# Performance work log

Hardware: AMD Instinct MI355X
Metric: run time of the kernel (lower is better)

Reference implementation:

```python
import jax, jax.numpy as jnp
import numpy as np

N_NODES = 50000
N_EDGES = 800000
D_FEAT = 96


def setup_inputs() -> dict:
    key = jax.random.key(0)
    kx, ks, kd = jax.random.split(key, 3)
    x = jax.random.normal(kx, (N_NODES, D_FEAT), dtype=jnp.float32)
    src = jax.random.randint(ks, (N_EDGES,), 0, N_NODES, dtype=jnp.int64)
    dst = jax.random.randint(kd, (N_EDGES,), 0, N_NODES, dtype=jnp.int64)
    return {"x": x, "src": src, "dst": dst}


def reference(x, src, dst):
    n = x.shape[0]
    ones = jnp.ones(src.shape[0], dtype=x.dtype)
    # out-degree: edges leaving each node (src side)
    out_deg = jnp.clip(jax.ops.segment_sum(ones, src, num_segments=n), 1.0, None)
    # in-degree: edges arriving at each node (dst side)
    in_deg = jnp.clip(jax.ops.segment_sum(ones, dst, num_segments=n), 1.0, None)
    # pre-scale by out-degree^{-1/2}
    xs = x * (out_deg ** -0.5)[:, None]
    # copy_u + sum aggregation: sum messages from src into dst
    agg = jax.ops.segment_sum(xs[src], dst, num_segments=n)
    # post-scale by in-degree^{-1/2}
    return agg * (in_deg ** -0.5)[:, None]
```

## Files before the change

kernel.cpp:

```cpp
#include <hip/hip_runtime.h>


#define D_FEAT 96
#define CAP 64
#define PART_SHIFT 8
#define PNODES 256
#define NP_MAX 256
#define EPB 4096
#define EREG 4
#define PTHREADS 1024
#define OVF_CAP 8192

__device__ __forceinline__ unsigned short f2bf_rne(float f) {
    unsigned u = __float_as_uint(f);
    unsigned r = (u >> 16) & 1u;
    u += 0x7fffu + r;
    return (unsigned short)(u >> 16);
}


__global__ __launch_bounds__(PTHREADS) void partition_kernel(
        const int* __restrict__ src, const int* __restrict__ dst,
        int n_edges, int np, int stride,
        int* __restrict__ pcur_d, int* __restrict__ pcur_s,
        unsigned* __restrict__ pbuf_d, unsigned short* __restrict__ pbuf_s,
        int* __restrict__ ctr,
        int* __restrict__ povf_d, int* __restrict__ sovf_d) {
    __shared__ int hcd[NP_MAX], hcs[NP_MAX];
    __shared__ int bd[NP_MAX], bs_[NP_MAX];
    __shared__ int od[NP_MAX], os_[NP_MAX];
    const int base = blockIdx.x * EPB;

    for (int i = threadIdx.x; i < NP_MAX; i += PTHREADS) {
        hcd[i] = 0; hcs[i] = 0; od[i] = 0; os_[i] = 0;
    }
    __syncthreads();

    unsigned v[EREG];
    #pragma unroll
    for (int k = 0; k < EREG; ++k) {
        int i = base + (int)threadIdx.x + (k << 10);
        if (i < n_edges) {
            int s = src[i], d = dst[i];
            unsigned pv = (unsigned)d | ((unsigned)s << 16);
            v[k] = pv;
            atomicAdd(&hcd[d >> PART_SHIFT], 1);
            atomicAdd(&hcs[s >> PART_SHIFT], 1);
        }
    }
    __syncthreads();

    for (int p = threadIdx.x; p < np; p += PTHREADS) {
        int cd = hcd[p];
        bd[p] = cd ? atomicAdd(&pcur_d[p], cd) : 0;
        int cs = hcs[p];
        bs_[p] = cs ? atomicAdd(&pcur_s[p], cs) : 0;
    }
    __syncthreads();

    #pragma unroll
    for (int k = 0; k < EREG; ++k) {
        int i = base + (int)threadIdx.x + (k << 10);
        if (i < n_edges) {
            unsigned pv = v[k];
            int d = (int)(pv & 0xffffu);
            int s = (int)(pv >> 16);
            int pd = d >> PART_SHIFT;
            int j = bd[pd] + atomicAdd(&od[pd], 1);
            if (j < stride) pbuf_d[(size_t)pd * stride + j] = pv;
            else { int k2 = atomicAdd(&ctr[1], 1); if (k2 < OVF_CAP) povf_d[k2] = (int)pv; }
            int ps = s >> PART_SHIFT;
            int j2 = bs_[ps] + atomicAdd(&os_[ps], 1);
            if (j2 < stride) pbuf_s[(size_t)ps * stride + j2] = (unsigned short)s;
            else { int k3 = atomicAdd(&ctr[2], 1); if (k3 < OVF_CAP) sovf_d[k3] = s; }
        }
    }
}


__global__ __launch_bounds__(PTHREADS) void bincnt_kernel(
        const unsigned* __restrict__ pbuf_d, const int* __restrict__ pcur_d,
        const unsigned short* __restrict__ pbuf_s, const int* __restrict__ pcur_s,
        int stride, int n_nodes,
        const float* __restrict__ x, unsigned* __restrict__ xs,
        int* __restrict__ cursor, int* __restrict__ out_cnt,
        unsigned short* __restrict__ slots,
        int* __restrict__ ctr,
        const int* __restrict__ povf_d, const int* __restrict__ sovf_d,
        int* __restrict__ ovf_d) {
    __shared__ unsigned short lslots[PNODES * CAP];
    __shared__ int lcnt[PNODES];
    __shared__ int lout[PNODES];
    const int b = blockIdx.x;
    const int nbase = b << PART_SHIFT;
    const int nloc = min(PNODES, n_nodes - nbase);

    for (int i = threadIdx.x; i < PNODES; i += PTHREADS) { lcnt[i] = 0; lout[i] = 0; }
    __syncthreads();

    int n = pcur_d[b]; if (n > stride) n = stride;
    for (int i = threadIdx.x; i < n; i += PTHREADS) {
        unsigned pv = pbuf_d[(size_t)b * stride + i];
        int dl = (int)(pv & 0xffu);
        int s  = (int)(pv >> 16);
        int pos = atomicAdd(&lcnt[dl], 1);
        if (pos < CAP) lslots[dl * CAP + pos] = (unsigned short)s;
        else { int k = atomicAdd(&ctr[0], 1); if (k < OVF_CAP) ovf_d[k] = (int)pv; }
    }
    int n2 = pcur_s[b]; if (n2 > stride) n2 = stride;
    for (int i = threadIdx.x; i < n2; i += PTHREADS) {
        int s = (int)pbuf_s[(size_t)b * stride + i];
        atomicAdd(&lout[s & (PNODES - 1)], 1);
    }
    int npv = ctr[1];
    if (npv > 0) {
        if (npv > OVF_CAP) npv = OVF_CAP;
        for (int i = threadIdx.x; i < npv; i += PTHREADS) {
            unsigned pv = (unsigned)povf_d[i];
            int d = (int)(pv & 0xffffu);
            if ((d >> PART_SHIFT) == b) {
                int dl = d & (PNODES - 1);
                int pos = atomicAdd(&lcnt[dl], 1);
                if (pos < CAP) lslots[dl * CAP + pos] = (unsigned short)(pv >> 16);
                else { int k = atomicAdd(&ctr[0], 1); if (k < OVF_CAP) ovf_d[k] = (int)pv; }
            }
        }
    }
    int nsv = ctr[2];
    if (nsv > 0) {
        if (nsv > OVF_CAP) nsv = OVF_CAP;
        for (int i = threadIdx.x; i < nsv; i += PTHREADS) {
            int s = sovf_d[i];
            if ((s >> PART_SHIFT) == b) atomicAdd(&lout[s & (PNODES - 1)], 1);
        }
    }
    __syncthreads();

    for (int i = threadIdx.x; i < nloc; i += PTHREADS) {
        cursor[nbase + i]  = lcnt[i];
        out_cnt[nbase + i] = lout[i];
    }
    const unsigned* ls = (const unsigned*)lslots;
    unsigned* gs = (unsigned*)slots + (size_t)nbase * (CAP / 2);
    const int ncopy = nloc * (CAP / 2);
    for (int i = threadIdx.x; i < ncopy; i += PTHREADS) gs[i] = ls[i];

    const int ntot = nloc * 24;
    for (int i = threadIdx.x; i < ntot; i += PTHREADS) {
        int nd = i / 24;
        int j  = i - nd * 24;
        int c  = lout[nd];
        float w = rsqrtf((float)(c < 1 ? 1 : c));
        float4 vv = ((const float4*)(x + (size_t)(nbase + nd) * D_FEAT))[j];
        unsigned lo0 = f2bf_rne(vv.x * w), hi0 = f2bf_rne(vv.y * w);
        unsigned lo1 = f2bf_rne(vv.z * w), hi1 = f2bf_rne(vv.w * w);
        uint2 o;
        o.x = lo0 | (hi0 << 16);
        o.y = lo1 | (hi1 << 16);
        ((uint2*)(xs + (size_t)(nbase + nd) * 48))[j] = o;
    }
}


__global__ __launch_bounds__(256) void gather_kernel(
        const unsigned* __restrict__ xs,
        const unsigned short* __restrict__ slots,
        const int* __restrict__ cursor,
        const float* __restrict__ x,
        const int* __restrict__ out_cnt,
        const int* __restrict__ ctr,
        const int* __restrict__ ovf_d,
        float* __restrict__ out, int n_nodes) {
    int wid  = threadIdx.x >> 6;
    int lane = threadIdx.x & 63;
    int node = __builtin_amdgcn_readfirstlane(blockIdx.x * 4 + wid);
    if (node >= n_nodes) return;

    int cnt_all = __builtin_amdgcn_readfirstlane(cursor[node]);
    int cnt = cnt_all < CAP ? cnt_all : CAP;

    float accx = 0.f, accy = 0.f;
    const bool act = lane < 48;

    if (cnt > 0) {
        int idx  = lane < cnt ? lane : cnt - 1;
        int sval = (int)slots[node * CAP + idx];

        int e = 0;
        for (; e + 16 <= cnt; e += 16) {
            if (act) {
                unsigned u[16];
                #pragma unroll
                for (int k = 0; k < 16; ++k) {
                    int s = __builtin_amdgcn_readlane(sval, e + k);
                    u[k] = xs[s * 48 + lane];
                }
                #pragma unroll
                for (int k = 0; k < 16; ++k) {
                    accx += __uint_as_float(u[k] << 16);
                    accy += __uint_as_float(u[k] & 0xffff0000u);
                }
            }
        }
        for (; e + 4 <= cnt; e += 4) {
            if (act) {
                unsigned u[4];
                #pragma unroll
                for (int k = 0; k < 4; ++k) {
                    int s = __builtin_amdgcn_readlane(sval, e + k);
                    u[k] = xs[s * 48 + lane];
                }
                #pragma unroll
                for (int k = 0; k < 4; ++k) {
                    accx += __uint_as_float(u[k] << 16);
                    accy += __uint_as_float(u[k] & 0xffff0000u);
                }
            }
        }
        for (; e < cnt; ++e) {
            if (act) {
                int s = __builtin_amdgcn_readlane(sval, e);
                unsigned u0 = xs[s * 48 + lane];
                accx += __uint_as_float(u0 << 16);
                accy += __uint_as_float(u0 & 0xffff0000u);
            }
        }
    }

    if (cnt_all > CAP) {
        int novf = __builtin_amdgcn_readfirstlane(ctr[0]);
        if (novf > OVF_CAP) novf = OVF_CAP;
        for (int k = 0; k < novf; ++k) {
            unsigned pv = (unsigned)ovf_d[k];
            if ((int)(pv & 0xffffu) == node) {
                int s = (int)(pv >> 16);
                int c = out_cnt[s];
                float w = rsqrtf((float)(c < 1 ? 1 : c));
                if (act) {
                    accx += w * x[(size_t)s * D_FEAT + lane * 2];
                    accy += w * x[(size_t)s * D_FEAT + lane * 2 + 1];
                }
            }
        }
    }

    float sc = rsqrtf((float)(cnt_all < 1 ? 1 : cnt_all));
    if (act) {
        float* op = out + (size_t)node * D_FEAT + lane * 2;
        op[0] = accx * sc;
        op[1] = accy * sc;
    }
}


__global__ void degree_kernel(const int* __restrict__ src,
                              const int* __restrict__ dst,
                              int* __restrict__ out_cnt,
                              int* __restrict__ in_cnt, int n_edges) {
    int i = blockIdx.x * blockDim.x + threadIdx.x;
    if (i < n_edges) {
        atomicAdd(&out_cnt[src[i]], 1);
        atomicAdd(&in_cnt[dst[i]], 1);
    }
}

__global__ void scale_kernel(float* __restrict__ osc, float* __restrict__ isc, int n) {
    int i = blockIdx.x * blockDim.x + threadIdx.x;
    if (i < n) {
        int c0 = ((const int*)osc)[i];
        int c1 = ((const int*)isc)[i];
        osc[i] = rsqrtf((float)(c0 < 1 ? 1 : c0));
        isc[i] = rsqrtf((float)(c1 < 1 ? 1 : c1));
    }
}

__global__ void scatter_kernel(const float* __restrict__ x,
                               const int* __restrict__ src,
                               const int* __restrict__ dst,
                               const float* __restrict__ osc,
                               const float* __restrict__ isc,
                               float* __restrict__ out, int n_edges) {
    int idx = blockIdx.x * blockDim.x + threadIdx.x;
    int e = idx / 24, c = idx % 24;
    if (e >= n_edges) return;
    int s = src[e], d = dst[e];
    float w = osc[s] * isc[d];
    const float4 v = *(const float4*)(x + (size_t)s * D_FEAT + c * 4);
    float* o = out + (size_t)d * D_FEAT + c * 4;
    unsafeAtomicAdd(o + 0, v.x * w);
    unsafeAtomicAdd(o + 1, v.y * w);
    unsafeAtomicAdd(o + 2, v.z * w);
    unsafeAtomicAdd(o + 3, v.w * w);
}


extern "C" void kernel_launch(void* const* d_in, const int* in_sizes, int n_in,
                              void* d_out, int out_size, void* d_ws, size_t ws_size,
                              hipStream_t stream) {
    const float* x  = (const float*)d_in[0];
    const int* src  = (const int*)d_in[1];
    const int* dst  = (const int*)d_in[2];
    float* out      = (float*)d_out;

    const int n_edges = in_sizes[1];
    const int n_nodes = in_sizes[0] / D_FEAT;

    const int np = (n_nodes + PNODES - 1) / PNODES;
    const int avg = n_edges / (np > 0 ? np : 1);
    const int stride = avg + avg / 4 + 1024;
    const int pblocks = (n_edges + EPB - 1) / EPB;

    const size_t pbuf_words  = (size_t)np * stride;
    const size_t pbufs_words = (pbuf_words + 1) / 2;

    int* pcur_d  = (int*)d_ws;
    int* pcur_s  = pcur_d + 256;
    int* ctr     = pcur_d + 512;
    int* ovf_d   = pcur_d + 1024;
    int* povf_d  = ovf_d + OVF_CAP;
    int* sovf_d  = povf_d + OVF_CAP;
    int* out_cnt = sovf_d + OVF_CAP;
    int* cursor  = out_cnt + 65536;
    unsigned* pbuf_dst = (unsigned*)(cursor + 65536);
    unsigned short* pbuf_src = (unsigned short*)(pbuf_dst + pbuf_words);
    unsigned* xs = pbuf_dst + pbuf_words + pbufs_words;
    unsigned short* slots = (unsigned short*)(xs + (size_t)n_nodes * 48);

    const size_t needed = ((size_t)1024 + 3 * OVF_CAP + 2 * 65536 + pbuf_words +
                           pbufs_words + (size_t)n_nodes * 48 +
                           (size_t)n_nodes * (CAP / 2)) * 4;

    if (ws_size >= needed && n_nodes <= 65536 && np <= NP_MAX && pblocks <= 256) {
        (void)hipMemsetAsync(d_ws, 0, 1024 * sizeof(int), stream);

        partition_kernel<<<pblocks, PTHREADS, 0, stream>>>(
            src, dst, n_edges, np, stride, pcur_d, pcur_s,
            pbuf_dst, pbuf_src, ctr, povf_d, sovf_d);

        bincnt_kernel<<<np, PTHREADS, 0, stream>>>(
            pbuf_dst, pcur_d, pbuf_src, pcur_s, stride, n_nodes,
            x, xs, cursor, out_cnt, slots, ctr, povf_d, sovf_d, ovf_d);

        gather_kernel<<<(n_nodes + 3) / 4, 256, 0, stream>>>(
            xs, slots, cursor, x, out_cnt, ctr, ovf_d, out, n_nodes);
    } else {
        float* osc = (float*)d_ws;
        float* isc = osc + 65536;
        (void)hipMemsetAsync(d_ws, 0, 2 * 65536 * sizeof(int), stream);
        (void)hipMemsetAsync(d_out, 0, (size_t)out_size * sizeof(float), stream);
        degree_kernel<<<(n_edges + 255) / 256, 256, 0, stream>>>(
            src, dst, (int*)osc, (int*)isc, n_edges);
        scale_kernel<<<(n_nodes + 255) / 256, 256, 0, stream>>>(osc, isc, n_nodes);
        const int total = n_edges * 24;
        scatter_kernel<<<(total + 255) / 256, 256, 0, stream>>>(
            x, src, dst, osc, isc, out, n_edges);
    }
}
```

Baseline: 128.3 us.

## Split gather into three feature-chunk launches with four edges per wavefront step

The gather kernel is split into three launches, each covering 32 of the 96 features. Within a wavefront, four groups of 16 lanes each process a different edge, and a cross-lane shuffle reduction combines the groups at the end. The goal is to shrink the working set of the bf16 feature table per pass so gathered rows stay in cache, and to keep all 64 lanes busy where only 48 were active before. Slot loads and output stores become nontemporal. In exchange, slot indices and cursors are read three times, two extra kernel launches are added, and every wavefront now pays for a shuffle reduction.

```diff
diff --git a/kernel.cpp b/kernel.cpp
--- a/kernel.cpp
+++ b/kernel.cpp
@@ -10,6 +10,8 @@
 #define EREG 4
 #define PTHREADS 1024
 #define OVF_CAP 8192
+
+typedef float vfloat2 __attribute__((ext_vector_type(2)));
 
 __device__ __forceinline__ unsigned short f2bf_rne(float f) {
     unsigned u = __float_as_uint(f);
@@ -162,7 +164,7 @@
 }
 
 
-__global__ __launch_bounds__(256) void gather_kernel(
+__global__ __launch_bounds__(256) void gatherc_kernel(
         const unsigned* __restrict__ xs,
         const unsigned short* __restrict__ slots,
         const int* __restrict__ cursor,
@@ -170,7 +172,7 @@
         const int* __restrict__ out_cnt,
         const int* __restrict__ ctr,
         const int* __restrict__ ovf_d,
-        float* __restrict__ out, int n_nodes) {
+        float* __restrict__ out, int n_nodes, int chunk) {
     int wid  = threadIdx.x >> 6;
     int lane = threadIdx.x & 63;
     int node = __builtin_amdgcn_readfirstlane(blockIdx.x * 4 + wid);
@@ -179,52 +181,48 @@
     int cnt_all = __builtin_amdgcn_readfirstlane(cursor[node]);
     int cnt = cnt_all < CAP ? cnt_all : CAP;
 
+    const int g = lane >> 4;
+    const int j = lane & 15;
+    const unsigned* __restrict__ xb = xs + chunk * 16;
+
     float accx = 0.f, accy = 0.f;
-    const bool act = lane < 48;
 
     if (cnt > 0) {
         int idx  = lane < cnt ? lane : cnt - 1;
-        int sval = (int)slots[node * CAP + idx];
+        int sval = (int)__builtin_nontemporal_load(&slots[node * CAP + idx]);
 
         int e = 0;
         for (; e + 16 <= cnt; e += 16) {
-            if (act) {
-                unsigned u[16];
-                #pragma unroll
-                for (int k = 0; k < 16; ++k) {
-                    int s = __builtin_amdgcn_readlane(sval, e + k);
-                    u[k] = xs[s * 48 + lane];
-                }
-                #pragma unroll
-                for (int k = 0; k < 16; ++k) {
-                    accx += __uint_as_float(u[k] << 16);
-                    accy += __uint_as_float(u[k] & 0xffff0000u);
-                }
+            unsigned u[4];
+            #pragma unroll
+            for (int k = 0; k < 4; ++k) {
+                int s = __shfl(sval, e + 4 * k + g, 64);
+                u[k] = xb[s * 48 + j];
             }
+            #pragma unroll
+            for (int k = 0; k < 4; ++k) {
+                accx += __uint_as_float(u[k] << 16);
+                accy += __uint_as_float(u[k] & 0xffff0000u);
+            }
         }
         for (; e + 4 <= cnt; e += 4) {
-            if (act) {
-                unsigned u[4];
-                #pragma unroll
-                for (int k = 0; k < 4; ++k) {
-                    int s = __builtin_amdgcn_readlane(sval, e + k);
-                    u[k] = xs[s * 48 + lane];
-                }
-                #pragma unroll
-                for (int k = 0; k < 4; ++k) {
-                    accx += __uint_as_float(u[k] << 16);
-                    accy += __uint_as_float(u[k] & 0xffff0000u);
-                }
-            }
-        }
-        for (; e < cnt; ++e) {
-            if (act) {
-                int s = __builtin_amdgcn_readlane(sval, e);
-                unsigned u0 = xs[s * 48 + lane];
-                accx += __uint_as_float(u0 << 16);
-                accy += __uint_as_float(u0 & 0xffff0000u);
-            }
-        }
+            int s = __shfl(sval, e + g, 64);
+            unsigned u = xb[s * 48 + j];
+            accx += __uint_as_float(u << 16);
+            accy += __uint_as_float(u & 0xffff0000u);
+        }
+        if (e < cnt) {
+            int eg = e + g;
+            bool valid = eg < cnt;
+            int s = __shfl(sval, valid ? eg : 0, 64);
+            unsigned u = valid ? xb[s * 48 + j] : 0u;
+            accx += __uint_as_float(u << 16);
+            accy += __uint_as_float(u & 0xffff0000u);
+        }
+        accx += __shfl_xor(accx, 32, 64);
+        accy += __shfl_xor(accy, 32, 64);
+        accx += __shfl_xor(accx, 16, 64);
+        accy += __shfl_xor(accy, 16, 64);
     }
 
     if (cnt_all > CAP) {
@@ -236,19 +234,21 @@
                 int s = (int)(pv >> 16);
                 int c = out_cnt[s];
                 float w = rsqrtf((float)(c < 1 ? 1 : c));
-                if (act) {
-                    accx += w * x[(size_t)s * D_FEAT + lane * 2];
-                    accy += w * x[(size_t)s * D_FEAT + lane * 2 + 1];
+                if (lane < 16) {
+                    accx += w * x[(size_t)s * D_FEAT + chunk * 32 + j * 2];
+                    accy += w * x[(size_t)s * D_FEAT + chunk * 32 + j * 2 + 1];
                 }
             }
         }
     }
 
     float sc = rsqrtf((float)(cnt_all < 1 ? 1 : cnt_all));
-    if (act) {
-        float* op = out + (size_t)node * D_FEAT + lane * 2;
-        op[0] = accx * sc;
-        op[1] = accy * sc;
+    if (lane < 16) {
+        vfloat2 o2;
+        o2.x = accx * sc;
+        o2.y = accy * sc;
+        __builtin_nontemporal_store(o2,
+            (vfloat2*)(out + (size_t)node * D_FEAT + chunk * 32 + j * 2));
     }
 }
 
@@ -341,8 +341,10 @@
             pbuf_dst, pcur_d, pbuf_src, pcur_s, stride, n_nodes,
             x, xs, cursor, out_cnt, slots, ctr, povf_d, sovf_d, ovf_d);
 
-        gather_kernel<<<(n_nodes + 3) / 4, 256, 0, stream>>>(
-            xs, slots, cursor, x, out_cnt, ctr, ovf_d, out, n_nodes);
+        for (int c = 0; c < 3; ++c) {
+            gatherc_kernel<<<(n_nodes + 3) / 4, 256, 0, stream>>>(
+                xs, slots, cursor, x, out_cnt, ctr, ovf_d, out, n_nodes, c);
+        }
     } else {
         float* osc = (float*)d_ws;
         float* isc = osc + 65536;
```

New measurement: 159.5 us. 1.24x slower.

## Count out-degrees with direct global atomics instead of partitioned src buffer

Applied to the files above, without the earlier changes.

The source-side partition buffer, its per-partition histogram and its overflow path are removed. The partition kernel now counts out-degree with a global atomicAdd per edge into out_cnt, which is zeroed by a larger memset, and the bincnt kernel reads those counts straight into shared memory. This drops a scattered write pass and a read pass over the src buffer. In exchange there are 800k global atomics spread over 50k addresses, plus a larger memset.

```diff
diff --git a/kernel.cpp b/kernel.cpp
--- a/kernel.cpp
+++ b/kernel.cpp
@@ -22,17 +22,18 @@
 __global__ __launch_bounds__(PTHREADS) void partition_kernel(
         const int* __restrict__ src, const int* __restrict__ dst,
         int n_edges, int np, int stride,
-        int* __restrict__ pcur_d, int* __restrict__ pcur_s,
-        unsigned* __restrict__ pbuf_d, unsigned short* __restrict__ pbuf_s,
+        int* __restrict__ pcur_d,
+        unsigned* __restrict__ pbuf_d,
+        int* __restrict__ out_cnt,
         int* __restrict__ ctr,
-        int* __restrict__ povf_d, int* __restrict__ sovf_d) {
-    __shared__ int hcd[NP_MAX], hcs[NP_MAX];
-    __shared__ int bd[NP_MAX], bs_[NP_MAX];
-    __shared__ int od[NP_MAX], os_[NP_MAX];
+        int* __restrict__ povf_d) {
+    __shared__ int hcd[NP_MAX];
+    __shared__ int bd[NP_MAX];
+    __shared__ int od[NP_MAX];
     const int base = blockIdx.x * EPB;
 
     for (int i = threadIdx.x; i < NP_MAX; i += PTHREADS) {
-        hcd[i] = 0; hcs[i] = 0; od[i] = 0; os_[i] = 0;
+        hcd[i] = 0; od[i] = 0;
     }
     __syncthreads();
 
@@ -45,7 +46,7 @@
             unsigned pv = (unsigned)d | ((unsigned)s << 16);
             v[k] = pv;
             atomicAdd(&hcd[d >> PART_SHIFT], 1);
-            atomicAdd(&hcs[s >> PART_SHIFT], 1);
+            atomicAdd(&out_cnt[s], 1);
         }
     }
     __syncthreads();
@@ -53,8 +54,6 @@
     for (int p = threadIdx.x; p < np; p += PTHREADS) {
         int cd = hcd[p];
         bd[p] = cd ? atomicAdd(&pcur_d[p], cd) : 0;
-        int cs = hcs[p];
-        bs_[p] = cs ? atomicAdd(&pcur_s[p], cs) : 0;
     }
     __syncthreads();
 
@@ -64,15 +63,10 @@
         if (i < n_edges) {
             unsigned pv = v[k];
             int d = (int)(pv & 0xffffu);
-            int s = (int)(pv >> 16);
             int pd = d >> PART_SHIFT;
             int j = bd[pd] + atomicAdd(&od[pd], 1);
             if (j < stride) pbuf_d[(size_t)pd * stride + j] = pv;
             else { int k2 = atomicAdd(&ctr[1], 1); if (k2 < OVF_CAP) povf_d[k2] = (int)pv; }
-            int ps = s >> PART_SHIFT;
-            int j2 = bs_[ps] + atomicAdd(&os_[ps], 1);
-            if (j2 < stride) pbuf_s[(size_t)ps * stride + j2] = (unsigned short)s;
-            else { int k3 = atomicAdd(&ctr[2], 1); if (k3 < OVF_CAP) sovf_d[k3] = s; }
         }
     }
 }
@@ -80,13 +74,12 @@
 
 __global__ __launch_bounds__(PTHREADS) void bincnt_kernel(
         const unsigned* __restrict__ pbuf_d, const int* __restrict__ pcur_d,
-        const unsigned short* __restrict__ pbuf_s, const int* __restrict__ pcur_s,
         int stride, int n_nodes,
         const float* __restrict__ x, unsigned* __restrict__ xs,
-        int* __restrict__ cursor, int* __restrict__ out_cnt,
+        int* __restrict__ cursor, const int* __restrict__ out_cnt,
         unsigned short* __restrict__ slots,
         int* __restrict__ ctr,
-        const int* __restrict__ povf_d, const int* __restrict__ sovf_d,
+        const int* __restrict__ povf_d,
         int* __restrict__ ovf_d) {
     __shared__ unsigned short lslots[PNODES * CAP];
     __shared__ int lcnt[PNODES];
@@ -95,7 +88,10 @@
     const int nbase = b << PART_SHIFT;
     const int nloc = min(PNODES, n_nodes - nbase);
 
-    for (int i = threadIdx.x; i < PNODES; i += PTHREADS) { lcnt[i] = 0; lout[i] = 0; }
+    for (int i = threadIdx.x; i < PNODES; i += PTHREADS) {
+        lcnt[i] = 0;
+        lout[i] = (i < nloc) ? out_cnt[nbase + i] : 0;
+    }
     __syncthreads();
 
     int n = pcur_d[b]; if (n > stride) n = stride;
@@ -106,11 +102,6 @@
         int pos = atomicAdd(&lcnt[dl], 1);
         if (pos < CAP) lslots[dl * CAP + pos] = (unsigned short)s;
         else { int k = atomicAdd(&ctr[0], 1); if (k < OVF_CAP) ovf_d[k] = (int)pv; }
-    }
-    int n2 = pcur_s[b]; if (n2 > stride) n2 = stride;
-    for (int i = threadIdx.x; i < n2; i += PTHREADS) {
-        int s = (int)pbuf_s[(size_t)b * stride + i];
-        atomicAdd(&lout[s & (PNODES - 1)], 1);
     }
     int npv = ctr[1];
     if (npv > 0) {
@@ -126,19 +117,10 @@
             }
         }
     }
-    int nsv = ctr[2];
-    if (nsv > 0) {
-        if (nsv > OVF_CAP) nsv = OVF_CAP;
-        for (int i = threadIdx.x; i < nsv; i += PTHREADS) {
-            int s = sovf_d[i];
-            if ((s >> PART_SHIFT) == b) atomicAdd(&lout[s & (PNODES - 1)], 1);
-        }
-    }
     __syncthreads();
 
     for (int i = threadIdx.x; i < nloc; i += PTHREADS) {
-        cursor[nbase + i]  = lcnt[i];
-        out_cnt[nbase + i] = lout[i];
+        cursor[nbase + i] = lcnt[i];
     }
     const unsigned* ls = (const unsigned*)lslots;
     unsigned* gs = (unsigned*)slots + (size_t)nbase * (CAP / 2);
@@ -310,36 +292,32 @@
     const int stride = avg + avg / 4 + 1024;
     const int pblocks = (n_edges + EPB - 1) / EPB;
 
-    const size_t pbuf_words  = (size_t)np * stride;
-    const size_t pbufs_words = (pbuf_words + 1) / 2;
+    const size_t pbuf_words = (size_t)np * stride;
 
     int* pcur_d  = (int*)d_ws;
-    int* pcur_s  = pcur_d + 256;
     int* ctr     = pcur_d + 512;
-    int* ovf_d   = pcur_d + 1024;
+    int* out_cnt = pcur_d + 1024;
+    int* ovf_d   = out_cnt + 65536;
     int* povf_d  = ovf_d + OVF_CAP;
-    int* sovf_d  = povf_d + OVF_CAP;
-    int* out_cnt = sovf_d + OVF_CAP;
-    int* cursor  = out_cnt + 65536;
+    int* cursor  = povf_d + OVF_CAP;
     unsigned* pbuf_dst = (unsigned*)(cursor + 65536);
-    unsigned short* pbuf_src = (unsigned short*)(pbuf_dst + pbuf_words);
-    unsigned* xs = pbuf_dst + pbuf_words + pbufs_words;
+    unsigned* xs = pbuf_dst + pbuf_words;
     unsigned short* slots = (unsigned short*)(xs + (size_t)n_nodes * 48);
 
-    const size_t needed = ((size_t)1024 + 3 * OVF_CAP + 2 * 65536 + pbuf_words +
-                           pbufs_words + (size_t)n_nodes * 48 +
+    const size_t needed = ((size_t)1024 + 2 * 65536 + 2 * OVF_CAP + pbuf_words +
+                           (size_t)n_nodes * 48 +
                            (size_t)n_nodes * (CAP / 2)) * 4;
 
     if (ws_size >= needed && n_nodes <= 65536 && np <= NP_MAX && pblocks <= 256) {
-        (void)hipMemsetAsync(d_ws, 0, 1024 * sizeof(int), stream);
+        (void)hipMemsetAsync(d_ws, 0, (1024 + 65536) * sizeof(int), stream);
 
         partition_kernel<<<pblocks, PTHREADS, 0, stream>>>(
-            src, dst, n_edges, np, stride, pcur_d, pcur_s,
-            pbuf_dst, pbuf_src, ctr, povf_d, sovf_d);
+            src, dst, n_edges, np, stride, pcur_d,
+            pbuf_dst, out_cnt, ctr, povf_d);
 
         bincnt_kernel<<<np, PTHREADS, 0, stream>>>(
-            pbuf_dst, pcur_d, pbuf_src, pcur_s, stride, n_nodes,
-            x, xs, cursor, out_cnt, slots, ctr, povf_d, sovf_d, ovf_d);
+            pbuf_dst, pcur_d, stride, n_nodes,
+            x, xs, cursor, out_cnt, slots, ctr, povf_d, ovf_d);
 
         gather_kernel<<<(n_nodes + 3) / 4, 256, 0, stream>>>(
             xs, slots, cursor, x, out_cnt, ctr, ovf_d, out, n_nodes);
```

Result: slower. 149.6 us (+16.6%).
